# Performance work log

Hardware: AMD Instinct MI355X
Metric: run time of the kernel (lower is better)

## Reference

```python
import jax, jax.numpy as jnp
import numpy as np

EXPAND = 2  # expand_ratio: head dim


def setup_inputs() -> dict:
    key = jax.random.key(0)
    k1, k2, k3 = jax.random.split(key, 3)
    n, b, d = 4096, 8, 1024
    x = jax.random.normal(k1, (n, b, d), dtype=jnp.float32)
    lower_bound = jnp.zeros((d,), dtype=jnp.float32)
    W_in = jax.random.normal(k2, (d, 3 * d), dtype=jnp.float32) / np.sqrt(d)
    W_out = jax.random.normal(k3, (d, d), dtype=jnp.float32) / np.sqrt(d)
    return {"x": x, "lower_bound": lower_bound, "W_in": W_in, "W_out": W_out}


def reference(x, lower_bound, W_in, W_out):
    # x: (n, b, d) sequence-first
    n, b, d = x.shape
    e = EXPAND
    h = d // e
    feat = x @ W_in                                  # (n, b, 3d)
    V, Q, Fg = jnp.split(feat, 3, axis=-1)
    V = jax.nn.gelu(V, approximate=False)            # nn.GELU default = exact erf
    Q = jax.nn.gelu(Q, approximate=False)
    Fg = jax.nn.sigmoid(Fg)
    V = V.reshape(n, b, h, e)
    Q = Q.reshape(n, b, h, e)
    Fg = Fg.reshape(n, b, h, e)
    lb = lower_bound.reshape(h, e)
    lam = lb + (1.0 - lb) * Fg                       # decay gate in (lb, 1)
    K = 1.0 - lam
    # GLA recurrence: S_t = diag(lam_t) S_{t-1} + k_t v_t^T ; o_t = q_t S_t
    # (exp(log_lambda) == lambda, so log-space decay collapses to direct multiply)
    def step(S, inp):
        lam_t, k_t, v_t, q_t = inp                   # each (b, h, e)
        S = lam_t[..., :, None] * S + k_t[..., :, None] * v_t[..., None, :]
        o_t = jnp.einsum('bhk,bhkv->bhv', q_t, S)
        return S, o_t
    S0 = jnp.zeros((b, h, e, e), dtype=x.dtype)
    _, o = jax.lax.scan(step, S0, (lam, K, V, Q))    # o: (n, b, h, e)
    o = o.reshape(n, b, d)
    return o @ W_out
```

## Files before the change

### kernel.cpp

```cpp
#include <hip/hip_runtime.h>
#include <hip/hip_bf16.h>
#include <math.h>

using frag8 = __attribute__((ext_vector_type(8))) short;
using f32x4 = __attribute__((ext_vector_type(4))) float;

#define BM 128
#define BN 128
#define BK 64

typedef const __attribute__((address_space(1))) unsigned char glb_u8;
typedef __attribute__((address_space(3))) unsigned char lds_u8;

__device__ __forceinline__ float b2f(unsigned short v) {
    union { unsigned u; float f; } x; x.u = ((unsigned)v) << 16; return x.f;
}
__device__ __forceinline__ unsigned short f2b(float f) {
    union { float f; unsigned u; } x; x.f = f;
    unsigned u = x.u;
    u += 0x7fffu + ((u >> 16) & 1u);
    return (unsigned short)(u >> 16);
}

__global__ __launch_bounds__(256) void cast_kernel(const float* __restrict__ in,
                                                   unsigned short* __restrict__ out, long n) {
    long i = ((long)blockIdx.x * 256 + threadIdx.x) * 8;
    if (i >= n) return;
    float4 a = *(const float4*)(in + i);
    float4 b = *(const float4*)(in + i + 4);
    struct alignas(16) U8 { unsigned short s[8]; } o;
    o.s[0] = f2b(a.x); o.s[1] = f2b(a.y); o.s[2] = f2b(a.z); o.s[3] = f2b(a.w);
    o.s[4] = f2b(b.x); o.s[5] = f2b(b.y); o.s[6] = f2b(b.z); o.s[7] = f2b(b.w);
    *(U8*)(out + i) = o;
}

__global__ void transpose_cast(const float* __restrict__ in, unsigned short* __restrict__ out,
                               int R, int Ccols) {
    __shared__ float tile[32][33];
    int bx = blockIdx.x * 32;
    int by = blockIdx.y * 32;
    int tx = threadIdx.x, ty = threadIdx.y;
    for (int r = ty; r < 32; r += 8)
        tile[r][tx] = in[(size_t)(by + r) * Ccols + bx + tx];
    __syncthreads();
    for (int r = ty; r < 32; r += 8)
        out[(size_t)(bx + r) * R + by + tx] = f2b(tile[tx][r]);
}

__global__ __launch_bounds__(256) void gemm_bf16(
    const unsigned short* __restrict__ A, const unsigned short* __restrict__ Bt,
    int M, int N, int K, int mode,
    float* __restrict__ Cf,
    unsigned short* __restrict__ Vp, unsigned short* __restrict__ Qp,
    unsigned short* __restrict__ Lp, const float* __restrict__ lb) {
    __shared__ __align__(16) unsigned short sA[BM * BK];
    __shared__ __align__(16) unsigned short sB[BN * BK];
    const int tid = threadIdx.x;
    const int lane16 = tid & 15;
    const int quad = (tid & 63) >> 4;
    const int wave = tid >> 6;
    const int wm = (wave >> 1) * 64;
    const int wn = (wave & 1) * 64;
    const long m0 = (long)blockIdx.y * BM;
    const long n0 = (long)blockIdx.x * BN;
    const long K2 = (long)K * 2;

    long srcA[4], srcB[4];
    int ldsOff[4];
#pragma unroll
    for (int p = 0; p < 4; ++p) {
        int off = p * 4096 + tid * 16;
        int r = off >> 7;
        int c = (off >> 4) & 7;
        int sc = c ^ (r & 7);
        ldsOff[p] = off;
        srcA[p] = (long)r * K2 + (long)sc * 16;
        srcB[p] = srcA[p];
    }
    const char* Ab = (const char*)A + m0 * K2;
    const char* Bb = (const char*)Bt + n0 * K2;

    int ldsA[2][4], ldsB[2][4];
#pragma unroll
    for (int mf = 0; mf < 4; ++mf) {
        int rowA = wm + mf * 16 + lane16;
        int rowB = wn + mf * 16 + lane16;
#pragma unroll
        for (int ks = 0; ks < 2; ++ks) {
            int j = quad + 4 * ks;
            ldsA[ks][mf] = rowA * 64 + ((j ^ (rowA & 7)) * 8);
            ldsB[ks][mf] = rowB * 64 + ((j ^ (rowB & 7)) * 8);
        }
    }

    f32x4 acc[4][4];
#pragma unroll
    for (int i = 0; i < 4; ++i)
#pragma unroll
        for (int j = 0; j < 4; ++j) acc[i][j] = (f32x4){0.f, 0.f, 0.f, 0.f};

    for (int kt = 0; kt < K; kt += BK) {
        __syncthreads();
        long kb = (long)kt * 2;
#pragma unroll
        for (int p = 0; p < 4; ++p)
            __builtin_amdgcn_global_load_lds((glb_u8*)(Ab + srcA[p] + kb),
                                             (lds_u8*)((char*)sA + ldsOff[p]), 16, 0, 0);
#pragma unroll
        for (int p = 0; p < 4; ++p)
            __builtin_amdgcn_global_load_lds((glb_u8*)(Bb + srcB[p] + kb),
                                             (lds_u8*)((char*)sB + ldsOff[p]), 16, 0, 0);
        __syncthreads();

#pragma unroll
        for (int ks = 0; ks < 2; ++ks) {
            frag8 af[4], bfr[4];
#pragma unroll
            for (int mf = 0; mf < 4; ++mf) af[mf] = *(const frag8*)(sA + ldsA[ks][mf]);
#pragma unroll
            for (int nf = 0; nf < 4; ++nf) bfr[nf] = *(const frag8*)(sB + ldsB[ks][nf]);
#pragma unroll
            for (int mf = 0; mf < 4; ++mf)
#pragma unroll
                for (int nf = 0; nf < 4; ++nf)
                    acc[mf][nf] = __builtin_amdgcn_mfma_f32_16x16x32_bf16(af[mf], bfr[nf], acc[mf][nf], 0, 0, 0);
        }
    }

    if (mode == 0) {
#pragma unroll
        for (int mf = 0; mf < 4; ++mf)
#pragma unroll
            for (int nf = 0; nf < 4; ++nf) {
                long col = n0 + wn + nf * 16 + lane16;
#pragma unroll
                for (int r = 0; r < 4; ++r) {
                    long row = m0 + wm + mf * 16 + quad * 4 + r;
                    Cf[row * N + col] = acc[mf][nf][r];
                }
            }
    } else {
        const int seg = (int)(n0 >> 10);
        const int cbase = (int)(n0 & 1023) + wn;
        unsigned short* dst = (seg == 0) ? Vp : (seg == 1 ? Qp : Lp);
#pragma unroll
        for (int mf = 0; mf < 4; ++mf)
#pragma unroll
            for (int nf = 0; nf < 4; ++nf) {
                int col = cbase + nf * 16 + lane16;
#pragma unroll
                for (int r = 0; r < 4; ++r) {
                    long row = m0 + wm + mf * 16 + quad * 4 + r;
                    float v = acc[mf][nf][r];
                    float res;
                    if (seg < 2) {
                        float u = 1.59576912f * v * (1.0f + 0.044715f * v * v);
                        res = v / (1.0f + __expf(-u));
                    } else {
                        float sg = 1.0f / (1.0f + __expf(-v));
                        float l = lb[col];
                        res = l + (1.0f - l) * sg;
                    }
                    dst[row * 1024 + col] = f2b(res);
                }
            }
    }
}

__global__ __launch_bounds__(256) void scan_phase1(
    const unsigned short* __restrict__ lam, const unsigned short* __restrict__ V,
    float* __restrict__ Sl, float* __restrict__ P, int L) {
    int cid = blockIdx.x * 256 + threadIdx.x;
    int c = blockIdx.y;
    int bi = cid >> 9, h = cid & 511;
    float s00 = 0, s01 = 0, s10 = 0, s11 = 0, p0 = 1.f, p1 = 1.f;
    int t0 = c * L;
    const unsigned* lamp = (const unsigned*)lam;
    const unsigned* vp = (const unsigned*)V;
    for (int t = t0; t < t0 + L; ++t) {
        long idx = (long)(t * 8 + bi) * 512 + h;
        unsigned lu = lamp[idx], vu = vp[idx];
        float la0 = b2f((unsigned short)lu), la1 = b2f((unsigned short)(lu >> 16));
        float v0 = b2f((unsigned short)vu), v1 = b2f((unsigned short)(vu >> 16));
        float k0 = 1.f - la0, k1 = 1.f - la1;
        s00 = fmaf(la0, s00, k0 * v0); s01 = fmaf(la0, s01, k0 * v1);
        s10 = fmaf(la1, s10, k1 * v0); s11 = fmaf(la1, s11, k1 * v1);
        p0 *= la0; p1 *= la1;
    }
    long base = (long)c * 4096 + cid;
    ((float4*)Sl)[base] = make_float4(s00, s01, s10, s11);
    ((float2*)P)[base] = make_float2(p0, p1);
}

__global__ __launch_bounds__(256) void scan_phase2(
    const float* __restrict__ Sl, const float* __restrict__ P,
    float* __restrict__ Sini, int C) {
    int idx = blockIdx.x * 256 + threadIdx.x;
    int cid = idx >> 2, ij = idx & 3, i = (idx >> 1) & 1;
    float s = 0.f;
    for (int c = 0; c < C; ++c) {
        long base = (long)c * 4096 + cid;
        Sini[base * 4 + ij] = s;
        s = fmaf(P[base * 2 + i], s, Sl[base * 4 + ij]);
    }
}

__global__ __launch_bounds__(256) void scan_phase3(
    const unsigned short* __restrict__ lam, const unsigned short* __restrict__ V,
    const unsigned short* __restrict__ Q, const float* __restrict__ Sini,
    unsigned short* __restrict__ o, int L) {
    int cid = blockIdx.x * 256 + threadIdx.x;
    int c = blockIdx.y;
    int bi = cid >> 9, h = cid & 511;
    float4 si = ((const float4*)Sini)[(long)c * 4096 + cid];
    float s00 = si.x, s01 = si.y, s10 = si.z, s11 = si.w;
    int t0 = c * L;
    const unsigned* lamp = (const unsigned*)lam;
    const unsigned* vp = (const unsigned*)V;
    const unsigned* qp = (const unsigned*)Q;
    unsigned* op = (unsigned*)o;
    for (int t = t0; t < t0 + L; ++t) {
        long idx = (long)(t * 8 + bi) * 512 + h;
        unsigned lu = lamp[idx], vu = vp[idx], qu = qp[idx];
        float la0 = b2f((unsigned short)lu), la1 = b2f((unsigned short)(lu >> 16));
        float v0 = b2f((unsigned short)vu), v1 = b2f((unsigned short)(vu >> 16));
        float q0 = b2f((unsigned short)qu), q1 = b2f((unsigned short)(qu >> 16));
        float k0 = 1.f - la0, k1 = 1.f - la1;
        s00 = fmaf(la0, s00, k0 * v0); s01 = fmaf(la0, s01, k0 * v1);
        s10 = fmaf(la1, s10, k1 * v0); s11 = fmaf(la1, s11, k1 * v1);
        float o0 = q0 * s00 + q1 * s10;
        float o1 = q0 * s01 + q1 * s11;
        op[idx] = (unsigned)f2b(o0) | ((unsigned)f2b(o1) << 16);
    }
}

extern "C" void kernel_launch(void* const* d_in, const int* in_sizes, int n_in,
                              void* d_out, int out_size, void* d_ws, size_t ws_size,
                              hipStream_t stream) {
    const float* x = (const float*)d_in[0];
    const float* lb = (const float*)d_in[1];
    const float* W_in = (const float*)d_in[2];
    const float* W_out = (const float*)d_in[3];
    float* out = (float*)d_out;

    const int n = 4096, b = 8, d = 1024;
    const long NB = (long)n * b;
    const int C = 64, L = 64;

    char* ws = (char*)d_ws;
    size_t off = 0;
    auto alloc = [&](size_t bytes) -> char* {
        char* p = ws + off;
        off += (bytes + 255) & ~(size_t)255;
        return p;
    };
    unsigned short* xb   = (unsigned short*)alloc(NB * d * 2);
    unsigned short* Wint = (unsigned short*)alloc((size_t)3 * d * d * 2);
    unsigned short* Wot  = (unsigned short*)alloc((size_t)d * d * 2);
    unsigned short* Vb   = (unsigned short*)alloc(NB * d * 2);
    unsigned short* Qb   = (unsigned short*)alloc(NB * d * 2);
    unsigned short* Lb   = (unsigned short*)alloc(NB * d * 2);
    float* Sl   = (float*)alloc((size_t)C * 4096 * 4 * 4);
    float* P    = (float*)alloc((size_t)C * 4096 * 2 * 4);
    float* Sini = (float*)alloc((size_t)C * 4096 * 4 * 4);

    cast_kernel<<<dim3((unsigned)((NB * d) / (256 * 8))), 256, 0, stream>>>(x, xb, NB * d);
    transpose_cast<<<dim3(3 * d / 32, d / 32), dim3(32, 8), 0, stream>>>(W_in, Wint, d, 3 * d);
    transpose_cast<<<dim3(d / 32, d / 32), dim3(32, 8), 0, stream>>>(W_out, Wot, d, d);
    gemm_bf16<<<dim3(3 * d / BN, (unsigned)(NB / BM)), 256, 0, stream>>>(
        xb, Wint, (int)NB, 3 * d, d, 1, nullptr, Vb, Qb, Lb, lb);
    scan_phase1<<<dim3(16, C), 256, 0, stream>>>(Lb, Vb, Sl, P, L);
    scan_phase2<<<dim3(64), 256, 0, stream>>>(Sl, P, Sini, C);
    unsigned short* ob = xb;
    scan_phase3<<<dim3(16, C), 256, 0, stream>>>(Lb, Vb, Qb, Sini, ob, L);
    gemm_bf16<<<dim3(d / BN, (unsigned)(NB / BM)), 256, 0, stream>>>(
        ob, Wot, (int)NB, d, d, 0, out, nullptr, nullptr, nullptr, nullptr);
}
```

Before: 790.4 us.

## Double-buffer GEMM LDS tiles and remap blocks per XCD for L2 locality

The bf16 GEMM now uses two LDS buffers per operand, prefetching the next K tile while MFMAs consume the current one. This drops one barrier per iteration and hides global-load latency. The grid becomes 1D, with block IDs remapped so each XCD works on a contiguous band of M rows and reuses A tiles in its L2. Launch bounds ask for 2 blocks per CU, which caps registers, and LDS use doubles to 64KB per block, which may limit occupancy.

```diff
diff --git a/kernel.cpp b/kernel.cpp
--- a/kernel.cpp
+++ b/kernel.cpp
@@ -47,25 +47,32 @@
         out[(size_t)(bx + r) * R + by + tx] = f2b(tile[tx][r]);
 }
 
-__global__ __launch_bounds__(256) void gemm_bf16(
+__global__ __launch_bounds__(256, 2) void gemm_bf16(
     const unsigned short* __restrict__ A, const unsigned short* __restrict__ Bt,
     int M, int N, int K, int mode,
     float* __restrict__ Cf,
     unsigned short* __restrict__ Vp, unsigned short* __restrict__ Qp,
     unsigned short* __restrict__ Lp, const float* __restrict__ lb) {
-    __shared__ __align__(16) unsigned short sA[BM * BK];
-    __shared__ __align__(16) unsigned short sB[BN * BK];
+    __shared__ __align__(16) unsigned short sA[2 * BM * BK];
+    __shared__ __align__(16) unsigned short sB[2 * BN * BK];
     const int tid = threadIdx.x;
     const int lane16 = tid & 15;
     const int quad = (tid & 63) >> 4;
     const int wave = tid >> 6;
     const int wm = (wave >> 1) * 64;
     const int wn = (wave & 1) * 64;
-    const long m0 = (long)blockIdx.y * BM;
-    const long n0 = (long)blockIdx.x * BN;
+
+    const int MT = M / BM, NT = N / BN;
+    const int bid = blockIdx.x;
+    const int xcd = bid & 7;
+    const int j = bid >> 3;
+    const int mt = xcd * (MT >> 3) + j / NT;
+    const int nt = j % NT;
+    const long m0 = (long)mt * BM;
+    const long n0 = (long)nt * BN;
     const long K2 = (long)K * 2;
 
-    long srcA[4], srcB[4];
+    long srcAB[4];
     int ldsOff[4];
 #pragma unroll
     for (int p = 0; p < 4; ++p) {
@@ -74,8 +81,7 @@
         int c = (off >> 4) & 7;
         int sc = c ^ (r & 7);
         ldsOff[p] = off;
-        srcA[p] = (long)r * K2 + (long)sc * 16;
-        srcB[p] = srcA[p];
+        srcAB[p] = (long)r * K2 + (long)sc * 16;
     }
     const char* Ab = (const char*)A + m0 * K2;
     const char* Bb = (const char*)Bt + n0 * K2;
@@ -87,9 +93,9 @@
         int rowB = wn + mf * 16 + lane16;
 #pragma unroll
         for (int ks = 0; ks < 2; ++ks) {
-            int j = quad + 4 * ks;
-            ldsA[ks][mf] = rowA * 64 + ((j ^ (rowA & 7)) * 8);
-            ldsB[ks][mf] = rowB * 64 + ((j ^ (rowB & 7)) * 8);
+            int jj = quad + 4 * ks;
+            ldsA[ks][mf] = rowA * 64 + ((jj ^ (rowA & 7)) * 8);
+            ldsB[ks][mf] = rowB * 64 + ((jj ^ (rowB & 7)) * 8);
         }
     }
 
@@ -97,28 +103,38 @@
 #pragma unroll
     for (int i = 0; i < 4; ++i)
 #pragma unroll
-        for (int j = 0; j < 4; ++j) acc[i][j] = (f32x4){0.f, 0.f, 0.f, 0.f};
-
-    for (int kt = 0; kt < K; kt += BK) {
+        for (int jj = 0; jj < 4; ++jj) acc[i][jj] = (f32x4){0.f, 0.f, 0.f, 0.f};
+
+    const int NIT = K / BK;
+#pragma unroll
+    for (int p = 0; p < 4; ++p) {
+        __builtin_amdgcn_global_load_lds((glb_u8*)(Ab + srcAB[p]),
+                                         (lds_u8*)((char*)sA + ldsOff[p]), 16, 0, 0);
+        __builtin_amdgcn_global_load_lds((glb_u8*)(Bb + srcAB[p]),
+                                         (lds_u8*)((char*)sB + ldsOff[p]), 16, 0, 0);
+    }
+
+    for (int it = 0; it < NIT; ++it) {
         __syncthreads();
-        long kb = (long)kt * 2;
-#pragma unroll
-        for (int p = 0; p < 4; ++p)
-            __builtin_amdgcn_global_load_lds((glb_u8*)(Ab + srcA[p] + kb),
-                                             (lds_u8*)((char*)sA + ldsOff[p]), 16, 0, 0);
-#pragma unroll
-        for (int p = 0; p < 4; ++p)
-            __builtin_amdgcn_global_load_lds((glb_u8*)(Bb + srcB[p] + kb),
-                                             (lds_u8*)((char*)sB + ldsOff[p]), 16, 0, 0);
-        __syncthreads();
-
+        if (it + 1 < NIT) {
+            long kb = (long)(it + 1) * BK * 2;
+            int bo = ((it + 1) & 1) * 16384;
+#pragma unroll
+            for (int p = 0; p < 4; ++p) {
+                __builtin_amdgcn_global_load_lds((glb_u8*)(Ab + srcAB[p] + kb),
+                                                 (lds_u8*)((char*)sA + bo + ldsOff[p]), 16, 0, 0);
+                __builtin_amdgcn_global_load_lds((glb_u8*)(Bb + srcAB[p] + kb),
+                                                 (lds_u8*)((char*)sB + bo + ldsOff[p]), 16, 0, 0);
+            }
+        }
+        const int bs = (it & 1) * 8192;
 #pragma unroll
         for (int ks = 0; ks < 2; ++ks) {
             frag8 af[4], bfr[4];
 #pragma unroll
-            for (int mf = 0; mf < 4; ++mf) af[mf] = *(const frag8*)(sA + ldsA[ks][mf]);
-#pragma unroll
-            for (int nf = 0; nf < 4; ++nf) bfr[nf] = *(const frag8*)(sB + ldsB[ks][nf]);
+            for (int mf = 0; mf < 4; ++mf) af[mf] = *(const frag8*)(sA + bs + ldsA[ks][mf]);
+#pragma unroll
+            for (int nf = 0; nf < 4; ++nf) bfr[nf] = *(const frag8*)(sB + bs + ldsB[ks][nf]);
 #pragma unroll
             for (int mf = 0; mf < 4; ++mf)
 #pragma unroll
@@ -267,12 +283,12 @@
     cast_kernel<<<dim3((unsigned)((NB * d) / (256 * 8))), 256, 0, stream>>>(x, xb, NB * d);
     transpose_cast<<<dim3(3 * d / 32, d / 32), dim3(32, 8), 0, stream>>>(W_in, Wint, d, 3 * d);
     transpose_cast<<<dim3(d / 32, d / 32), dim3(32, 8), 0, stream>>>(W_out, Wot, d, d);
-    gemm_bf16<<<dim3(3 * d / BN, (unsigned)(NB / BM)), 256, 0, stream>>>(
+    gemm_bf16<<<dim3((unsigned)((NB / BM) * (3 * d / BN))), 256, 0, stream>>>(
         xb, Wint, (int)NB, 3 * d, d, 1, nullptr, Vb, Qb, Lb, lb);
     scan_phase1<<<dim3(16, C), 256, 0, stream>>>(Lb, Vb, Sl, P, L);
     scan_phase2<<<dim3(64), 256, 0, stream>>>(Sl, P, Sini, C);
     unsigned short* ob = xb;
     scan_phase3<<<dim3(16, C), 256, 0, stream>>>(Lb, Vb, Qb, Sini, ob, L);
-    gemm_bf16<<<dim3(d / BN, (unsigned)(NB / BM)), 256, 0, stream>>>(
+    gemm_bf16<<<dim3((unsigned)((NB / BM) * (d / BN))), 256, 0, stream>>>(
         ob, Wot, (int)NB, d, d, 0, out, nullptr, nullptr, nullptr, nullptr);
 }
```

Result: no change. 793.9 us (+0.4%).
